# Kernel optimization log

Hardware: AMD Instinct MI355X
Metric: run time of the kernel (lower is better)

## Reference

```python
import jax, jax.numpy as jnp
import numpy as np

N_NODES = 100000

def gcn_conv(x, edge_index, W, b):
    # GCNConv with normalize=True and self-loops:
    # out = D^{-1/2} (A + I) D^{-1/2} (x W) + b
    h = x @ W                                   # [N, out]
    src, dst = edge_index[0], edge_index[1]
    deg = jax.ops.segment_sum(jnp.ones(src.shape[0], h.dtype), dst,
                              num_segments=N_NODES) + 1.0  # +1 for self loop
    dinv = jax.lax.rsqrt(deg)
    norm = dinv[src] * dinv[dst]                # [E]
    agg = jax.ops.segment_sum(h[src] * norm[:, None], dst,
                              num_segments=N_NODES)        # [N, out]
    agg = agg + h * (1.0 / deg)[:, None]        # self-loop term: norm_ii = 1/deg_i
    return agg + b


def setup_inputs() -> dict:
    key = jax.random.key(0)
    k0, k1, k2, k3 = jax.random.split(key, 4)
    N, E, F_IN, H, C = N_NODES, 1600000, 256, 128, 40
    x = jax.random.normal(k0, (N, F_IN), dtype=jnp.float32)
    edge_index = jax.random.randint(k1, (2, E), 0, N, dtype=jnp.int64)
    W1 = jax.random.normal(k2, (F_IN, H), dtype=jnp.float32) * (1.0 / np.sqrt(F_IN))
    b1 = jnp.zeros((H,), jnp.float32)
    W2 = jax.random.normal(k3, (H, C), dtype=jnp.float32) * (1.0 / np.sqrt(H))
    b2 = jnp.zeros((C,), jnp.float32)
    return {"x": x, "edge_index": edge_index, "W1": W1, "b1": b1, "W2": W2, "b2": b2}


def reference(x, edge_index, W1, b1, W2, b2):
    # layer 1 + ReLU (dropout = identity in eval mode)
    h = jax.nn.relu(gcn_conv(x, edge_index, W1, b1))
    # final layer (no activation)
    return gcn_conv(h, edge_index, W2, b2)
```

## Files before the change

kernel.cpp:

```cpp
#include <hip/hip_runtime.h>
#include <hip/hip_bf16.h>


#define FIN 256
#define HDIM 128
#define CDIM 40
#define CAP 8192
#define EC 2048

typedef __attribute__((ext_vector_type(8))) short bf16x8;
typedef __attribute__((ext_vector_type(4))) float f32x4;

__device__ inline short f2bf(float f) {
    unsigned u = __float_as_uint(f);
    unsigned r = (u + 0x7FFFu + ((u >> 16) & 1u)) >> 16;
    return (short)r;
}
__device__ inline float bflo(unsigned u) { return __uint_as_float(u << 16); }
__device__ inline float bfhi(unsigned u) { return __uint_as_float(u & 0xFFFF0000u); }

__global__ __launch_bounds__(256) void p1_hist_k(const int* __restrict__ ei, int* __restrict__ mat,
                                                 int E, int NBUCK) {
    __shared__ int hist[512];
    for (int t = threadIdx.x; t < NBUCK; t += 256) hist[t] = 0;
    __syncthreads();
    int e0 = blockIdx.x * EC;
#pragma unroll
    for (int k = 0; k < EC; k += 256) {
        int e = e0 + k + threadIdx.x;
        if (e < E) atomicAdd(&hist[ei[E + e] >> 8], 1);
    }
    __syncthreads();
    for (int t = threadIdx.x; t < NBUCK; t += 256) mat[blockIdx.x * NBUCK + t] = hist[t];
}

__global__ __launch_bounds__(64) void scan_cols_k(int* __restrict__ mat, int* __restrict__ bcnt,
                                                  int NB1, int NBUCK) {
    int b = blockIdx.x;
    int lane = threadIdx.x;
    int carry = b * CAP;
    for (int c0 = 0; c0 < NB1; c0 += 64) {
        int idx = c0 + lane;
        int v = (idx < NB1) ? mat[idx * NBUCK + b] : 0;
        int incl = v;
#pragma unroll
        for (int off = 1; off < 64; off <<= 1) {
            int t = __shfl_up(incl, off);
            if (lane >= off) incl += t;
        }
        if (idx < NB1) mat[idx * NBUCK + b] = carry + (incl - v);
        carry += __shfl(incl, 63);
    }
    if (lane == 0) bcnt[b] = carry - b * CAP;
}

__global__ __launch_bounds__(256) void p1_scatter_k(const int* __restrict__ ei, const int* __restrict__ mat,
                                                    int* __restrict__ bmem, int E, int NBUCK) {
    __shared__ int base[512];
    for (int t = threadIdx.x; t < NBUCK; t += 256) base[t] = mat[blockIdx.x * NBUCK + t];
    __syncthreads();
    int e0 = blockIdx.x * EC;
#pragma unroll
    for (int k = 0; k < EC; k += 256) {
        int e = e0 + k + threadIdx.x;
        if (e < E) {
            int s = ei[e];
            int d = ei[E + e];
            int pos = atomicAdd(&base[d >> 8], 1);
            bmem[pos] = s | ((d & 255) << 20);
        }
    }
}

__global__ __launch_bounds__(256) void p2_build_k(const int* __restrict__ bmem, const int* __restrict__ bcnt,
                                                  int* __restrict__ csr, int2* __restrict__ nseg,
                                                  float* __restrict__ dinv, float* __restrict__ invd, int N) {
    __shared__ int hist[256], cur[256], sc[256];
    __shared__ int stage[CAP];
    const int b = blockIdx.x;
    const int tid = threadIdx.x;
    int cnt = bcnt[b];
    if (cnt > CAP) cnt = CAP;
    const int* src = bmem + b * CAP;
    hist[tid] = 0;
    __syncthreads();
    for (int j = tid; j < cnt; j += 256) atomicAdd(&hist[src[j] >> 20], 1);
    __syncthreads();
    int v = hist[tid];
    sc[tid] = v;
    __syncthreads();
    for (int off = 1; off < 256; off <<= 1) {
        int t = (tid >= off) ? sc[tid - off] : 0;
        __syncthreads();
        sc[tid] += t;
        __syncthreads();
    }
    int excl = sc[tid] - v;
    cur[tid] = excl;
    int i = b * 256 + tid;
    if (i < N) {
        nseg[i] = make_int2(b * CAP + excl, v);
        float dg = (float)(v + 1);
        dinv[i] = rsqrtf(dg);
        invd[i] = 1.0f / dg;
    }
    __syncthreads();
    for (int j = tid; j < cnt; j += 256) {
        int rec = src[j];
        int pos = atomicAdd(&cur[rec >> 20], 1);
        stage[pos] = rec & 0xFFFFF;
    }
    __syncthreads();
    int* dst = csr + b * CAP;
    for (int j = tid; j < cnt; j += 256) dst[j] = stage[j];
}

__global__ __launch_bounds__(256) void castW1_k(const float* __restrict__ W1, short* __restrict__ W1T) {
    int idx = blockIdx.x * 256 + threadIdx.x;
    int k = idx >> 7, n = idx & 127;
    W1T[n * FIN + k] = f2bf(W1[idx]);
}

#define LDSTRIDE 40
__global__ __launch_bounds__(256) void gemm1_mfma_k(const float* __restrict__ X,
                                                    const short* __restrict__ W1T,
                                                    short* __restrict__ T1b, int N) {
    __shared__ short As[128 * LDSTRIDE];
    __shared__ short Bs[128 * LDSTRIDE];
    const int tid = threadIdx.x;
    const int lane = tid & 63;
    const int wid = tid >> 6;
    const int w0 = wid & 1, w1 = wid >> 1;
    const int quad = lane >> 4;
    const int l16 = lane & 15;
    const int rowbase = blockIdx.x * 128;
    const int sr = tid >> 1;
    const int sh = tid & 1;

    f32x4 acc[4][4];
#pragma unroll
    for (int a = 0; a < 4; a++)
#pragma unroll
        for (int b = 0; b < 4; b++) acc[a][b] = (f32x4){0.f, 0.f, 0.f, 0.f};

    const int arow = min(rowbase + sr, N - 1);
    const float* xsrc = X + (size_t)arow * FIN + sh * 16;
    const int4* bsrc = (const int4*)(W1T + (size_t)sr * FIN + sh * 16);

    for (int k0 = 0; k0 < FIN; k0 += 32) {
        float vals[16];
        *(float4*)&vals[0]  = *(const float4*)(xsrc + k0);
        *(float4*)&vals[4]  = *(const float4*)(xsrc + k0 + 4);
        *(float4*)&vals[8]  = *(const float4*)(xsrc + k0 + 8);
        *(float4*)&vals[12] = *(const float4*)(xsrc + k0 + 12);
        short tmp[16];
#pragma unroll
        for (int c = 0; c < 16; c++) tmp[c] = f2bf(vals[c]);
        ((int4*)&As[sr * LDSTRIDE + sh * 16])[0] = ((int4*)tmp)[0];
        ((int4*)&As[sr * LDSTRIDE + sh * 16])[1] = ((int4*)tmp)[1];
        int4 b0 = bsrc[k0 >> 3];
        int4 b1 = bsrc[(k0 >> 3) + 1];
        ((int4*)&Bs[sr * LDSTRIDE + sh * 16])[0] = b0;
        ((int4*)&Bs[sr * LDSTRIDE + sh * 16])[1] = b1;
        __syncthreads();

        bf16x8 afr[4], bfr[4];
#pragma unroll
        for (int mt = 0; mt < 4; mt++)
            afr[mt] = *(const bf16x8*)&As[(w1 * 64 + mt * 16 + l16) * LDSTRIDE + quad * 8];
#pragma unroll
        for (int nt = 0; nt < 4; nt++)
            bfr[nt] = *(const bf16x8*)&Bs[(w0 * 64 + nt * 16 + l16) * LDSTRIDE + quad * 8];
#pragma unroll
        for (int mt = 0; mt < 4; mt++)
#pragma unroll
            for (int nt = 0; nt < 4; nt++)
                acc[mt][nt] = __builtin_amdgcn_mfma_f32_16x16x32_bf16(afr[mt], bfr[nt], acc[mt][nt], 0, 0, 0);
        __syncthreads();
    }
#pragma unroll
    for (int mt = 0; mt < 4; mt++) {
#pragma unroll
        for (int r = 0; r < 4; r++) {
            int row = rowbase + w1 * 64 + mt * 16 + quad * 4 + r;
            if (row < N) {
#pragma unroll
                for (int nt = 0; nt < 4; nt++) {
                    int col = w0 * 64 + nt * 16 + l16;
                    T1b[(size_t)row * HDIM + col] = f2bf(acc[mt][nt][r]);
                }
            }
        }
    }
}

__global__ __launch_bounds__(256) void agg1_k(const short* __restrict__ T1b, const int2* __restrict__ nseg,
                                              const int* __restrict__ csr, const float* __restrict__ dinv,
                                              const float* __restrict__ invd, const float* __restrict__ b1,
                                              float* __restrict__ H, int N) {
    const int lane = threadIdx.x & 63;
    const int i = blockIdx.x * 4 + (threadIdx.x >> 6);
    if (i >= N) return;
    const int2 sg = nseg[i];
    const int e0 = sg.x, deg = sg.y;
    int sv = 0; float wv = 0.f;
    if (lane < deg) { sv = csr[e0 + lane]; wv = dinv[sv]; }

    float accx = 0.f, accy = 0.f;
    const int dmain = deg < 64 ? deg : 64;
    const int d4 = dmain & ~3;
    const unsigned* rowp = (const unsigned*)T1b;
    int j = 0;
    for (; j < d4; j += 4) {
        int s0 = __shfl(sv, j), s1 = __shfl(sv, j + 1), s2 = __shfl(sv, j + 2), s3 = __shfl(sv, j + 3);
        float w0 = __shfl(wv, j), w1 = __shfl(wv, j + 1), w2 = __shfl(wv, j + 2), w3 = __shfl(wv, j + 3);
        unsigned r0 = rowp[(size_t)s0 * 64 + lane];
        unsigned r1 = rowp[(size_t)s1 * 64 + lane];
        unsigned r2 = rowp[(size_t)s2 * 64 + lane];
        unsigned r3 = rowp[(size_t)s3 * 64 + lane];
        accx += w0 * bflo(r0) + w1 * bflo(r1) + w2 * bflo(r2) + w3 * bflo(r3);
        accy += w0 * bfhi(r0) + w1 * bfhi(r1) + w2 * bfhi(r2) + w3 * bfhi(r3);
    }
    for (; j < dmain; ++j) {
        int s = __shfl(sv, j); float w = __shfl(wv, j);
        unsigned r = rowp[(size_t)s * 64 + lane];
        accx += w * bflo(r); accy += w * bfhi(r);
    }
    for (int e = e0 + 64; e < e0 + deg; ++e) {
        int s = csr[e]; float w = dinv[s];
        unsigned r = rowp[(size_t)s * 64 + lane];
        accx += w * bflo(r); accy += w * bfhi(r);
    }
    const float di = dinv[i], sf = invd[i];
    unsigned rs = rowp[(size_t)i * 64 + lane];
    float2 bc = *(const float2*)(b1 + 2 * lane);
    float ox = bc.x + sf * bflo(rs) + di * accx;
    float oy = bc.y + sf * bfhi(rs) + di * accy;
    float2 o = {fmaxf(ox, 0.f), fmaxf(oy, 0.f)};
    *(float2*)(H + (size_t)i * HDIM + 2 * lane) = o;
}

__global__ __launch_bounds__(256) void gemm2_k(const float* __restrict__ Hm, const float* __restrict__ W,
                                               float* __restrict__ T, int N) {
    __shared__ float As2[32][128];
    __shared__ float Bs2[32][40];
    const int tid = threadIdx.x;
    const int ct = tid & 7;
    const int rt = tid >> 3;
    const int rowbase = blockIdx.x * 128;
    float acc[4][5];
#pragma unroll
    for (int i = 0; i < 4; i++)
#pragma unroll
        for (int j = 0; j < 5; j++) acc[i][j] = 0.0f;

    for (int k0 = 0; k0 < HDIM; k0 += 32) {
#pragma unroll
        for (int l = 0; l < 4; ++l) {
            int idx = tid + l * 256;
            int r = idx >> 3;
            int kc = (idx & 7) * 4;
            int gr = min(rowbase + r, N - 1);
            float4 v = *(const float4*)(Hm + (size_t)gr * HDIM + k0 + kc);
            As2[kc + 0][r] = v.x; As2[kc + 1][r] = v.y;
            As2[kc + 2][r] = v.z; As2[kc + 3][r] = v.w;
        }
#pragma unroll
        for (int l = 0; l < 5; ++l) {
            int idx = tid + l * 256;
            Bs2[idx / 40][idx % 40] = W[k0 * 40 + idx];
        }
        __syncthreads();
#pragma unroll
        for (int kk = 0; kk < 32; ++kk) {
            float4 av = *(const float4*)&As2[kk][rt * 4];
            float a[4] = {av.x, av.y, av.z, av.w};
            float b[5];
#pragma unroll
            for (int j = 0; j < 5; j++) b[j] = Bs2[kk][ct * 5 + j];
#pragma unroll
            for (int i = 0; i < 4; i++)
#pragma unroll
                for (int j = 0; j < 5; j++) acc[i][j] += a[i] * b[j];
        }
        __syncthreads();
    }
#pragma unroll
    for (int i = 0; i < 4; i++) {
        int r = rowbase + rt * 4 + i;
        if (r < N) {
#pragma unroll
            for (int j = 0; j < 5; j++) T[(size_t)r * CDIM + ct * 5 + j] = acc[i][j];
        }
    }
}

__global__ __launch_bounds__(256) void agg2_k(const float* __restrict__ T2, const int2* __restrict__ nseg,
                                              const int* __restrict__ csr, const float* __restrict__ dinv,
                                              const float* __restrict__ invd, const float* __restrict__ b2,
                                              float* __restrict__ OUT, int N) {
    const int lane = threadIdx.x & 63;
    const int i = blockIdx.x * 4 + (threadIdx.x >> 6);
    if (i >= N) return;
    const int2 sg = nseg[i];
    const int e0 = sg.x, deg = sg.y;
    int sv = 0; float wv = 0.f;
    if (lane < deg) { sv = csr[e0 + lane]; wv = dinv[sv]; }
    const int c = lane < CDIM ? lane : CDIM - 1;
    float accE = 0.f;
    const int dmain = deg < 64 ? deg : 64;
    const int d4 = dmain & ~3;
    int j = 0;
    for (; j < d4; j += 4) {
        int s0 = __shfl(sv, j), s1 = __shfl(sv, j + 1), s2 = __shfl(sv, j + 2), s3 = __shfl(sv, j + 3);
        float w0 = __shfl(wv, j), w1 = __shfl(wv, j + 1), w2 = __shfl(wv, j + 2), w3 = __shfl(wv, j + 3);
        float v0 = T2[(size_t)s0 * CDIM + c];
        float v1 = T2[(size_t)s1 * CDIM + c];
        float v2 = T2[(size_t)s2 * CDIM + c];
        float v3 = T2[(size_t)s3 * CDIM + c];
        accE += w0 * v0 + w1 * v1 + w2 * v2 + w3 * v3;
    }
    for (; j < dmain; ++j) {
        int s = __shfl(sv, j); float w = __shfl(wv, j);
        accE += w * T2[(size_t)s * CDIM + c];
    }
    for (int e = e0 + 64; e < e0 + deg; ++e) {
        int s = csr[e]; float w = dinv[s];
        accE += w * T2[(size_t)s * CDIM + c];
    }
    if (lane < CDIM)
        OUT[(size_t)i * CDIM + lane] = b2[lane] + invd[i] * T2[(size_t)i * CDIM + lane] + dinv[i] * accE;
}

extern "C" void kernel_launch(void* const* d_in, const int* in_sizes, int n_in,
                              void* d_out, int out_size, void* d_ws, size_t ws_size,
                              hipStream_t stream) {
    const float* x   = (const float*)d_in[0];
    const int*   ei  = (const int*)d_in[1];
    const float* W1  = (const float*)d_in[2];
    const float* b1  = (const float*)d_in[3];
    const float* W2  = (const float*)d_in[4];
    const float* b2  = (const float*)d_in[5];
    float*       out = (float*)d_out;

    const int Hd  = in_sizes[3];
    const int Fin = in_sizes[2] / Hd;
    const int N   = in_sizes[0] / Fin;
    const int E   = in_sizes[1] / 2;

    const int NBUCK = (N + 255) / 256;
    const int NB1   = (E + EC - 1) / EC;

    char* base = (char*)d_ws;
    size_t off = 0;
    auto alloc = [&](size_t bytes) -> void* {
        void* p = base + off;
        off += (bytes + 255) & ~(size_t)255;
        return p;
    };
    size_t matB  = (size_t)NB1 * NBUCK * 4;
    size_t bmemB = (size_t)NBUCK * CAP * 4;
    size_t t1bB  = (size_t)N * HDIM * 2;
    size_t regA  = matB + 256 + bmemB;
    if (t1bB > regA) regA = t1bB;
    char* pA = (char*)alloc(regA);
    int*   mat  = (int*)pA;
    int*   bmem = (int*)(pA + ((matB + 255) & ~(size_t)255));
    short* t1b  = (short*)pA;

    int*   bcnt = (int*)alloc((size_t)NBUCK * 4);
    int*   csr  = (int*)alloc((size_t)NBUCK * CAP * 4);
    int2*  nseg = (int2*)alloc((size_t)N * 8);
    float* dinv = (float*)alloc((size_t)N * 4);
    float* invd = (float*)alloc((size_t)N * 4);
    short* W1T  = (short*)alloc((size_t)HDIM * FIN * 2);
    float* h    = (float*)alloc((size_t)N * HDIM * 4);
    float* t2   = (float*)alloc((size_t)N * CDIM * 4);

    p1_hist_k<<<NB1, 256, 0, stream>>>(ei, mat, E, NBUCK);
    scan_cols_k<<<NBUCK, 64, 0, stream>>>(mat, bcnt, NB1, NBUCK);
    p1_scatter_k<<<NB1, 256, 0, stream>>>(ei, mat, bmem, E, NBUCK);
    p2_build_k<<<NBUCK, 256, 0, stream>>>(bmem, bcnt, csr, nseg, dinv, invd, N);
    castW1_k<<<(HDIM * Fin + 255) / 256, 256, 0, stream>>>(W1, W1T);

    gemm1_mfma_k<<<(N + 127) / 128, 256, 0, stream>>>(x, W1T, t1b, N);
    agg1_k<<<(N + 3) / 4, 256, 0, stream>>>(t1b, nseg, csr, dinv, invd, b1, h, N);
    gemm2_k<<<(N + 127) / 128, 256, 0, stream>>>(h, W2, t2, N);
    agg2_k<<<(N + 3) / 4, 256, 0, stream>>>(t2, nseg, csr, dinv, invd, b2, out, N);
}
```

Measured before the change: 394.5 us.

## Store layer-1 output in bf16, use MFMA for second GEMM, widen gathers

The layer-1 aggregation now writes its ReLU output packed as bf16 rather than fp32, which halves the intermediate traffic. The second GEMM becomes an MFMA bf16 kernel with W2 transposed and padded to 48 columns. Both aggregation kernels unroll their gather loops to 8 edges and use readlane instead of shuffles to broadcast neighbour indices and weights. The partitioning kernels switch to 1024-thread blocks with 8192 edges per block. The added bf16 rounding of the hidden activations slightly reduces precision.

Result: faster. 360.6 us (-8.6%).

```diff
diff --git a/kernel.cpp b/kernel.cpp
--- a/kernel.cpp
+++ b/kernel.cpp
@@ -6,7 +6,7 @@
 #define HDIM 128
 #define CDIM 40
 #define CAP 8192
-#define EC 2048
+#define EC 8192
 
 typedef __attribute__((ext_vector_type(8))) short bf16x8;
 typedef __attribute__((ext_vector_type(4))) float f32x4;
@@ -18,20 +18,24 @@
 }
 __device__ inline float bflo(unsigned u) { return __uint_as_float(u << 16); }
 __device__ inline float bfhi(unsigned u) { return __uint_as_float(u & 0xFFFF0000u); }
-
-__global__ __launch_bounds__(256) void p1_hist_k(const int* __restrict__ ei, int* __restrict__ mat,
-                                                 int E, int NBUCK) {
+__device__ inline int rdl_i(int v, int l) { return __builtin_amdgcn_readlane(v, l); }
+__device__ inline float rdl_f(float v, int l) {
+    return __uint_as_float((unsigned)__builtin_amdgcn_readlane((int)__float_as_uint(v), l));
+}
+
+__global__ __launch_bounds__(1024) void p1_hist_k(const int* __restrict__ ei, int* __restrict__ mat,
+                                                  int E, int NBUCK) {
     __shared__ int hist[512];
-    for (int t = threadIdx.x; t < NBUCK; t += 256) hist[t] = 0;
+    for (int t = threadIdx.x; t < NBUCK; t += 1024) hist[t] = 0;
     __syncthreads();
     int e0 = blockIdx.x * EC;
 #pragma unroll
-    for (int k = 0; k < EC; k += 256) {
+    for (int k = 0; k < EC; k += 1024) {
         int e = e0 + k + threadIdx.x;
         if (e < E) atomicAdd(&hist[ei[E + e] >> 8], 1);
     }
     __syncthreads();
-    for (int t = threadIdx.x; t < NBUCK; t += 256) mat[blockIdx.x * NBUCK + t] = hist[t];
+    for (int t = threadIdx.x; t < NBUCK; t += 1024) mat[blockIdx.x * NBUCK + t] = hist[t];
 }
 
 __global__ __launch_bounds__(64) void scan_cols_k(int* __restrict__ mat, int* __restrict__ bcnt,
@@ -54,14 +58,14 @@
     if (lane == 0) bcnt[b] = carry - b * CAP;
 }
 
-__global__ __launch_bounds__(256) void p1_scatter_k(const int* __restrict__ ei, const int* __restrict__ mat,
-                                                    int* __restrict__ bmem, int E, int NBUCK) {
+__global__ __launch_bounds__(1024) void p1_scatter_k(const int* __restrict__ ei, const int* __restrict__ mat,
+                                                     int* __restrict__ bmem, int E, int NBUCK) {
     __shared__ int base[512];
-    for (int t = threadIdx.x; t < NBUCK; t += 256) base[t] = mat[blockIdx.x * NBUCK + t];
+    for (int t = threadIdx.x; t < NBUCK; t += 1024) base[t] = mat[blockIdx.x * NBUCK + t];
     __syncthreads();
     int e0 = blockIdx.x * EC;
 #pragma unroll
-    for (int k = 0; k < EC; k += 256) {
+    for (int k = 0; k < EC; k += 1024) {
         int e = e0 + k + threadIdx.x;
         if (e < E) {
             int s = ei[e];
@@ -119,6 +123,12 @@
     int idx = blockIdx.x * 256 + threadIdx.x;
     int k = idx >> 7, n = idx & 127;
     W1T[n * FIN + k] = f2bf(W1[idx]);
+}
+
+__global__ __launch_bounds__(256) void castW2_k(const float* __restrict__ W2, short* __restrict__ W2T) {
+    int idx = blockIdx.x * 256 + threadIdx.x;
+    int c = idx >> 7, k = idx & 127;
+    W2T[idx] = (c < CDIM) ? f2bf(W2[k * CDIM + c]) : (short)0;
 }
 
 #define LDSTRIDE 40
@@ -197,7 +207,7 @@
 __global__ __launch_bounds__(256) void agg1_k(const short* __restrict__ T1b, const int2* __restrict__ nseg,
                                               const int* __restrict__ csr, const float* __restrict__ dinv,
                                               const float* __restrict__ invd, const float* __restrict__ b1,
-                                              float* __restrict__ H, int N) {
+                                              unsigned* __restrict__ Hb, int N) {
     const int lane = threadIdx.x & 63;
     const int i = blockIdx.x * 4 + (threadIdx.x >> 6);
     if (i >= N) return;
@@ -208,21 +218,29 @@
 
     float accx = 0.f, accy = 0.f;
     const int dmain = deg < 64 ? deg : 64;
-    const int d4 = dmain & ~3;
+    const int d8 = dmain & ~7;
     const unsigned* rowp = (const unsigned*)T1b;
     int j = 0;
-    for (; j < d4; j += 4) {
-        int s0 = __shfl(sv, j), s1 = __shfl(sv, j + 1), s2 = __shfl(sv, j + 2), s3 = __shfl(sv, j + 3);
-        float w0 = __shfl(wv, j), w1 = __shfl(wv, j + 1), w2 = __shfl(wv, j + 2), w3 = __shfl(wv, j + 3);
+    for (; j < d8; j += 8) {
+        int   s0 = rdl_i(sv, j),     s1 = rdl_i(sv, j + 1), s2 = rdl_i(sv, j + 2), s3 = rdl_i(sv, j + 3);
+        int   s4 = rdl_i(sv, j + 4), s5 = rdl_i(sv, j + 5), s6 = rdl_i(sv, j + 6), s7 = rdl_i(sv, j + 7);
+        float w0 = rdl_f(wv, j),     w1 = rdl_f(wv, j + 1), w2 = rdl_f(wv, j + 2), w3 = rdl_f(wv, j + 3);
+        float w4 = rdl_f(wv, j + 4), w5 = rdl_f(wv, j + 5), w6 = rdl_f(wv, j + 6), w7 = rdl_f(wv, j + 7);
         unsigned r0 = rowp[(size_t)s0 * 64 + lane];
         unsigned r1 = rowp[(size_t)s1 * 64 + lane];
         unsigned r2 = rowp[(size_t)s2 * 64 + lane];
         unsigned r3 = rowp[(size_t)s3 * 64 + lane];
-        accx += w0 * bflo(r0) + w1 * bflo(r1) + w2 * bflo(r2) + w3 * bflo(r3);
-        accy += w0 * bfhi(r0) + w1 * bfhi(r1) + w2 * bfhi(r2) + w3 * bfhi(r3);
+        unsigned r4 = rowp[(size_t)s4 * 64 + lane];
+        unsigned r5 = rowp[(size_t)s5 * 64 + lane];
+        unsigned r6 = rowp[(size_t)s6 * 64 + lane];
+        unsigned r7 = rowp[(size_t)s7 * 64 + lane];
+        accx += w0 * bflo(r0) + w1 * bflo(r1) + w2 * bflo(r2) + w3 * bflo(r3)
+              + w4 * bflo(r4) + w5 * bflo(r5) + w6 * bflo(r6) + w7 * bflo(r7);
+        accy += w0 * bfhi(r0) + w1 * bfhi(r1) + w2 * bfhi(r2) + w3 * bfhi(r3)
+              + w4 * bfhi(r4) + w5 * bfhi(r5) + w6 * bfhi(r6) + w7 * bfhi(r7);
     }
     for (; j < dmain; ++j) {
-        int s = __shfl(sv, j); float w = __shfl(wv, j);
+        int s = rdl_i(sv, j); float w = rdl_f(wv, j);
         unsigned r = rowp[(size_t)s * 64 + lane];
         accx += w * bflo(r); accy += w * bfhi(r);
     }
@@ -234,63 +252,75 @@
     const float di = dinv[i], sf = invd[i];
     unsigned rs = rowp[(size_t)i * 64 + lane];
     float2 bc = *(const float2*)(b1 + 2 * lane);
-    float ox = bc.x + sf * bflo(rs) + di * accx;
-    float oy = bc.y + sf * bfhi(rs) + di * accy;
-    float2 o = {fmaxf(ox, 0.f), fmaxf(oy, 0.f)};
-    *(float2*)(H + (size_t)i * HDIM + 2 * lane) = o;
-}
-
-__global__ __launch_bounds__(256) void gemm2_k(const float* __restrict__ Hm, const float* __restrict__ W,
-                                               float* __restrict__ T, int N) {
-    __shared__ float As2[32][128];
-    __shared__ float Bs2[32][40];
+    float ox = fmaxf(bc.x + sf * bflo(rs) + di * accx, 0.f);
+    float oy = fmaxf(bc.y + sf * bfhi(rs) + di * accy, 0.f);
+    unsigned pk = ((unsigned)(unsigned short)f2bf(ox)) | (((unsigned)(unsigned short)f2bf(oy)) << 16);
+    Hb[(size_t)i * 64 + lane] = pk;
+}
+
+__global__ __launch_bounds__(256) void gemm2_mfma_k(const short* __restrict__ Hb,
+                                                    const short* __restrict__ W2T,
+                                                    float* __restrict__ T2, int N) {
+    __shared__ short As[128 * LDSTRIDE];
+    __shared__ short Bs[48 * LDSTRIDE];
     const int tid = threadIdx.x;
-    const int ct = tid & 7;
-    const int rt = tid >> 3;
+    const int lane = tid & 63;
+    const int wid = tid >> 6;
+    const int quad = lane >> 4;
+    const int l16 = lane & 15;
     const int rowbase = blockIdx.x * 128;
-    float acc[4][5];
-#pragma unroll
-    for (int i = 0; i < 4; i++)
-#pragma unroll
-        for (int j = 0; j < 5; j++) acc[i][j] = 0.0f;
+    const int sr = tid >> 1;
+    const int sh = tid & 1;
+
+    f32x4 acc[2][3];
+#pragma unroll
+    for (int a = 0; a < 2; a++)
+#pragma unroll
+        for (int b = 0; b < 3; b++) acc[a][b] = (f32x4){0.f, 0.f, 0.f, 0.f};
+
+    const int arow = min(rowbase + sr, N - 1);
+    const int4* asrc = (const int4*)(Hb + (size_t)arow * HDIM + sh * 16);
+    const int br = tid >> 1, bh = tid & 1;
+    const int4* bsrc = (const int4*)(W2T + br * HDIM + bh * 16);
 
     for (int k0 = 0; k0 < HDIM; k0 += 32) {
-#pragma unroll
-        for (int l = 0; l < 4; ++l) {
-            int idx = tid + l * 256;
-            int r = idx >> 3;
-            int kc = (idx & 7) * 4;
-            int gr = min(rowbase + r, N - 1);
-            float4 v = *(const float4*)(Hm + (size_t)gr * HDIM + k0 + kc);
-            As2[kc + 0][r] = v.x; As2[kc + 1][r] = v.y;
-            As2[kc + 2][r] = v.z; As2[kc + 3][r] = v.w;
+        int4 a0 = asrc[k0 >> 3];
+        int4 a1 = asrc[(k0 >> 3) + 1];
+        ((int4*)&As[sr * LDSTRIDE + sh * 16])[0] = a0;
+        ((int4*)&As[sr * LDSTRIDE + sh * 16])[1] = a1;
+        if (tid < 96) {
+            int4 b0 = bsrc[k0 >> 3];
+            int4 b1 = bsrc[(k0 >> 3) + 1];
+            ((int4*)&Bs[br * LDSTRIDE + bh * 16])[0] = b0;
+            ((int4*)&Bs[br * LDSTRIDE + bh * 16])[1] = b1;
         }
-#pragma unroll
-        for (int l = 0; l < 5; ++l) {
-            int idx = tid + l * 256;
-            Bs2[idx / 40][idx % 40] = W[k0 * 40 + idx];
-        }
-        __syncthreads();
-#pragma unroll
-        for (int kk = 0; kk < 32; ++kk) {
-            float4 av = *(const float4*)&As2[kk][rt * 4];
-            float a[4] = {av.x, av.y, av.z, av.w};
-            float b[5];
-#pragma unroll
-            for (int j = 0; j < 5; j++) b[j] = Bs2[kk][ct * 5 + j];
-#pragma unroll
-            for (int i = 0; i < 4; i++)
-#pragma unroll
-                for (int j = 0; j < 5; j++) acc[i][j] += a[i] * b[j];
-        }
-        __syncthreads();
-    }
-#pragma unroll
-    for (int i = 0; i < 4; i++) {
-        int r = rowbase + rt * 4 + i;
-        if (r < N) {
-#pragma unroll
-            for (int j = 0; j < 5; j++) T[(size_t)r * CDIM + ct * 5 + j] = acc[i][j];
+        __syncthreads();
+        bf16x8 afr[2], bfr[3];
+#pragma unroll
+        for (int mt = 0; mt < 2; mt++)
+            afr[mt] = *(const bf16x8*)&As[(wid * 32 + mt * 16 + l16) * LDSTRIDE + quad * 8];
+#pragma unroll
+        for (int nt = 0; nt < 3; nt++)
+            bfr[nt] = *(const bf16x8*)&Bs[(nt * 16 + l16) * LDSTRIDE + quad * 8];
+#pragma unroll
+        for (int mt = 0; mt < 2; mt++)
+#pragma unroll
+            for (int nt = 0; nt < 3; nt++)
+                acc[mt][nt] = __builtin_amdgcn_mfma_f32_16x16x32_bf16(afr[mt], bfr[nt], acc[mt][nt], 0, 0, 0);
+        __syncthreads();
+    }
+#pragma unroll
+    for (int mt = 0; mt < 2; mt++) {
+#pragma unroll
+        for (int r = 0; r < 4; r++) {
+            int row = rowbase + wid * 32 + mt * 16 + quad * 4 + r;
+            if (row < N) {
+#pragma unroll
+                for (int nt = 0; nt < 3; nt++) {
+                    int col = nt * 16 + l16;
+                    if (col < CDIM) T2[(size_t)row * CDIM + col] = acc[mt][nt][r];
+                }
+            }
         }
     }
 }
@@ -309,19 +339,25 @@
     const int c = lane < CDIM ? lane : CDIM - 1;
     float accE = 0.f;
     const int dmain = deg < 64 ? deg : 64;
-    const int d4 = dmain & ~3;
+    const int d8 = dmain & ~7;
     int j = 0;
-    for (; j < d4; j += 4) {
-        int s0 = __shfl(sv, j), s1 = __shfl(sv, j + 1), s2 = __shfl(sv, j + 2), s3 = __shfl(sv, j + 3);
-        float w0 = __shfl(wv, j), w1 = __shfl(wv, j + 1), w2 = __shfl(wv, j + 2), w3 = __shfl(wv, j + 3);
+    for (; j < d8; j += 8) {
+        int   s0 = rdl_i(sv, j),     s1 = rdl_i(sv, j + 1), s2 = rdl_i(sv, j + 2), s3 = rdl_i(sv, j + 3);
+        int   s4 = rdl_i(sv, j + 4), s5 = rdl_i(sv, j + 5), s6 = rdl_i(sv, j + 6), s7 = rdl_i(sv, j + 7);
+        float w0 = rdl_f(wv, j),     w1 = rdl_f(wv, j + 1), w2 = rdl_f(wv, j + 2), w3 = rdl_f(wv, j + 3);
+        float w4 = rdl_f(wv, j + 4), w5 = rdl_f(wv, j + 5), w6 = rdl_f(wv, j + 6), w7 = rdl_f(wv, j + 7);
         float v0 = T2[(size_t)s0 * CDIM + c];
         float v1 = T2[(size_t)s1 * CDIM + c];
         float v2 = T2[(size_t)s2 * CDIM + c];
         float v3 = T2[(size_t)s3 * CDIM + c];
-        accE += w0 * v0 + w1 * v1 + w2 * v2 + w3 * v3;
+        float v4 = T2[(size_t)s4 * CDIM + c];
+        float v5 = T2[(size_t)s5 * CDIM + c];
+        float v6 = T2[(size_t)s6 * CDIM + c];
+        float v7 = T2[(size_t)s7 * CDIM + c];
+        accE += w0 * v0 + w1 * v1 + w2 * v2 + w3 * v3 + w4 * v4 + w5 * v5 + w6 * v6 + w7 * v7;
     }
     for (; j < dmain; ++j) {
-        int s = __shfl(sv, j); float w = __shfl(wv, j);
+        int s = rdl_i(sv, j); float w = rdl_f(wv, j);
         accE += w * T2[(size_t)s * CDIM + c];
     }
     for (int e = e0 + 64; e < e0 + deg; ++e) {
@@ -368,23 +404,25 @@
     int*   bmem = (int*)(pA + ((matB + 255) & ~(size_t)255));
     short* t1b  = (short*)pA;
 
-    int*   bcnt = (int*)alloc((size_t)NBUCK * 4);
-    int*   csr  = (int*)alloc((size_t)NBUCK * CAP * 4);
-    int2*  nseg = (int2*)alloc((size_t)N * 8);
-    float* dinv = (float*)alloc((size_t)N * 4);
-    float* invd = (float*)alloc((size_t)N * 4);
-    short* W1T  = (short*)alloc((size_t)HDIM * FIN * 2);
-    float* h    = (float*)alloc((size_t)N * HDIM * 4);
-    float* t2   = (float*)alloc((size_t)N * CDIM * 4);
-
-    p1_hist_k<<<NB1, 256, 0, stream>>>(ei, mat, E, NBUCK);
+    int*      bcnt = (int*)alloc((size_t)NBUCK * 4);
+    int*      csr  = (int*)alloc((size_t)NBUCK * CAP * 4);
+    int2*     nseg = (int2*)alloc((size_t)N * 8);
+    float*    dinv = (float*)alloc((size_t)N * 4);
+    float*    invd = (float*)alloc((size_t)N * 4);
+    short*    W1T  = (short*)alloc((size_t)HDIM * FIN * 2);
+    short*    W2T  = (short*)alloc((size_t)48 * HDIM * 2);
+    unsigned* hb   = (unsigned*)alloc((size_t)N * HDIM * 2);
+    float*    t2   = (float*)alloc((size_t)N * CDIM * 4);
+
+    p1_hist_k<<<NB1, 1024, 0, stream>>>(ei, mat, E, NBUCK);
     scan_cols_k<<<NBUCK, 64, 0, stream>>>(mat, bcnt, NB1, NBUCK);
-    p1_scatter_k<<<NB1, 256, 0, stream>>>(ei, mat, bmem, E, NBUCK);
+    p1_scatter_k<<<NB1, 1024, 0, stream>>>(ei, mat, bmem, E, NBUCK);
     p2_build_k<<<NBUCK, 256, 0, stream>>>(bmem, bcnt, csr, nseg, dinv, invd, N);
     castW1_k<<<(HDIM * Fin + 255) / 256, 256, 0, stream>>>(W1, W1T);
+    castW2_k<<<(48 * HDIM + 255) / 256, 256, 0, stream>>>(W2, W2T);
 
     gemm1_mfma_k<<<(N + 127) / 128, 256, 0, stream>>>(x, W1T, t1b, N);
-    agg1_k<<<(N + 3) / 4, 256, 0, stream>>>(t1b, nseg, csr, dinv, invd, b1, h, N);
-    gemm2_k<<<(N + 127) / 128, 256, 0, stream>>>(h, W2, t2, N);
+    agg1_k<<<(N + 3) / 4, 256, 0, stream>>>(t1b, nseg, csr, dinv, invd, b1, hb, N);
+    gemm2_mfma_k<<<(N + 127) / 128, 256, 0, stream>>>((const short*)hb, W2T, t2, N);
     agg2_k<<<(N + 3) / 4, 256, 0, stream>>>(t2, nseg, csr, dinv, invd, b2, out, N);
 }
```
